# Kernel tuning notes

Hardware: AMD Instinct MI355X
Metric: run time of the kernel (lower is better)

Reference implementation:

```python
import jax, jax.numpy as jnp
import numpy as np

N_NODES = 100000
N_EDGES = 1600000
HIDDEN = 64
N_MID = 3  # num_layers=5 -> 1 first + 3 middle + 1 last


def setup_inputs() -> dict:
    key = jax.random.key(0)
    ks = jax.random.split(key, 12)
    x = jax.random.normal(ks[0], (N_NODES, 1), dtype=jnp.float32)
    edge_index = jax.random.randint(ks[1], (2, N_EDGES), 0, N_NODES, dtype=jnp.int32)
    edge_weight = jax.random.uniform(ks[2], (N_EDGES,), dtype=jnp.float32)
    s0 = 1.0  # fan_in=1
    sh = 1.0 / np.sqrt(HIDDEN)
    Wrel0 = jax.random.normal(ks[3], (HIDDEN, 1), dtype=jnp.float32) * s0
    brel0 = jax.random.normal(ks[4], (HIDDEN,), dtype=jnp.float32) * s0
    Wroot0 = jax.random.normal(ks[5], (HIDDEN, 1), dtype=jnp.float32) * s0
    Wrel_mid = jax.random.normal(ks[6], (N_MID, HIDDEN, HIDDEN), dtype=jnp.float32) * sh
    brel_mid = jax.random.normal(ks[7], (N_MID, HIDDEN), dtype=jnp.float32) * sh
    Wroot_mid = jax.random.normal(ks[8], (N_MID, HIDDEN, HIDDEN), dtype=jnp.float32) * sh
    WrelL = jax.random.normal(ks[9], (1, HIDDEN), dtype=jnp.float32) * sh
    brelL = jax.random.normal(ks[10], (1,), dtype=jnp.float32) * sh
    WrootL = jax.random.normal(ks[11], (1, HIDDEN), dtype=jnp.float32) * sh
    return {"x": x, "edge_index": edge_index, "edge_weight": edge_weight,
            "Wrel0": Wrel0, "brel0": brel0, "Wroot0": Wroot0,
            "Wrel_mid": Wrel_mid, "brel_mid": brel_mid, "Wroot_mid": Wroot_mid,
            "WrelL": WrelL, "brelL": brelL, "WrootL": WrootL}


def reference(x, edge_index, edge_weight, Wrel0, brel0, Wroot0,
              Wrel_mid, brel_mid, Wroot_mid, WrelL, brelL, WrootL):
    src = edge_index[0]
    dst = edge_index[1]
    n = x.shape[0]

    def conv(h, Wrel, brel, Wroot):
        # PyG GraphConv(aggr='add'): lin_rel(sum_j w_ij * h_j) + lin_root(h_i)
        msg = h[src] * edge_weight[:, None]          # [E, C]
        agg = jax.ops.segment_sum(msg, dst, num_segments=n)  # [N, C]
        return agg @ Wrel.T + brel + h @ Wroot.T

    # dropout omitted (deterministic reference); relu after all but last layer
    h = jax.nn.relu(conv(x, Wrel0, brel0, Wroot0))
    for i in range(Wrel_mid.shape[0]):
        h = jax.nn.relu(conv(h, Wrel_mid[i], brel_mid[i], Wroot_mid[i]))
    return conv(h, WrelL, brelL, WrootL)  # [N, 1]
```

## Files before the change

### kernel.cpp

```cpp
#include <hip/hip_runtime.h>
#include <stdint.h>


#define NN 100000
#define NE 1600000
#define HID 64
#define NBKT 391
#define CAP 8192
#define PMAX (NBKT * CAP)
#define TILE 4096
#define EPT 16
#define NTILE ((NE + TILE - 1) / TILE)

typedef __attribute__((ext_vector_type(8))) short bf16x8;
typedef __attribute__((ext_vector_type(4))) float f32x4;
typedef __attribute__((ext_vector_type(2))) unsigned int u32x2;
typedef __attribute__((ext_vector_type(4))) unsigned int u32x4;

__device__ __forceinline__ uint32_t rne_bf16(float v) {
    uint32_t u = __float_as_uint(v);
    return (u + 0x7fffu + ((u >> 16) & 1u)) >> 16;
}


__global__ __launch_bounds__(256) void k_bpart(const int* __restrict__ src,
                                               const int* __restrict__ dst,
                                               const float* __restrict__ w,
                                               int* __restrict__ bcur,
                                               int2* __restrict__ bpairs) {
    __shared__ int  hcnt[NBKT];
    __shared__ int  hoff[NBKT];
    __shared__ int  hadj[NBKT];
    __shared__ int  sc0[512];
    __shared__ int  sc1[512];
    __shared__ int2 sT[TILE];
    __shared__ int  sAdj[TILE];
    int tile0 = blockIdx.x * TILE;
    int t = threadIdx.x;
    for (int i = t; i < NBKT; i += 256) hcnt[i] = 0;
    __syncthreads();

    int   pk[EPT];
    int   bk[EPT];
    float wv[EPT];
    #pragma unroll
    for (int k = 0; k < EPT; k++) {
        int e = tile0 + t + k * 256;
        if (e < NE) {
            int d = dst[e];
            int b = d >> 8;
            pk[k] = (src[e] << 8) | (d & 255);
            wv[k] = w[e];
            bk[k] = b;
            atomicAdd(&hcnt[b], 1);
        } else {
            bk[k] = -1;
        }
    }
    __syncthreads();

    sc0[t]       = (t < NBKT) ? hcnt[t] : 0;
    sc0[t + 256] = (t + 256 < NBKT) ? hcnt[t + 256] : 0;
    __syncthreads();
    int* cur = sc0;
    int* oth = sc1;
    for (int off = 1; off < 512; off <<= 1) {
        int v0 = cur[t]       + ((t       >= off) ? cur[t - off]       : 0);
        int v1 = cur[t + 256] + ((t + 256 >= off) ? cur[t + 256 - off] : 0);
        oth[t] = v0;
        oth[t + 256] = v1;
        __syncthreads();
        int* tmp = cur; cur = oth; oth = tmp;
    }
    for (int i = t; i < NBKT; i += 256) {
        int c = hcnt[i];
        int excl = cur[i] - c;
        hoff[i] = excl;
        int gbase = c ? atomicAdd(&bcur[i], c) : 0;
        hadj[i] = gbase - excl;
        hcnt[i] = 0;
    }
    __syncthreads();

    #pragma unroll
    for (int k = 0; k < EPT; k++) {
        if (bk[k] >= 0) {
            int b = bk[k];
            int pos = hoff[b] + atomicAdd(&hcnt[b], 1);
            sT[pos] = make_int2(pk[k], __float_as_int(wv[k]));
            sAdj[pos] = hadj[b];
        }
    }
    __syncthreads();

    int n = NE - tile0; if (n > TILE) n = TILE;
    for (int j = t; j < n; j += 256)
        bpairs[sAdj[j] + j] = sT[j];
}

__global__ __launch_bounds__(256) void k_bcsr(const int* __restrict__ bcur,
                                              const int2* __restrict__ bpairs,
                                              int* __restrict__ offs,
                                              int* __restrict__ ends,
                                              uint32_t* __restrict__ pairs) {
    __shared__ int2 sE[CAP];
    __shared__ int cnt[256];
    __shared__ int scn[256];
    __shared__ int cur[256];
    int k = blockIdx.x, t = threadIdx.x;
    int base = k * CAP;
    int scnt = bcur[k] - base;
    cnt[t] = 0;
    __syncthreads();
    for (int j = t; j < scnt; j += 256) {
        int2 q = bpairs[base + j];
        sE[j] = q;
        atomicAdd(&cnt[q.x & 255], 1);
    }
    __syncthreads();
    int v = cnt[t], acc = v;
    scn[t] = v;
    __syncthreads();
    for (int off = 1; off < 256; off <<= 1) {
        int u = (t >= off) ? scn[t - off] : 0;
        __syncthreads();
        acc += u;
        scn[t] = acc;
        __syncthreads();
    }
    int excl = acc - v;
    cur[t] = excl;
    int d = (k << 8) + t;
    if (d < NN) {
        offs[d] = base + excl;
        ends[d] = base + excl + v;
    }
    __syncthreads();
    for (int j = t; j < scnt; j += 256) {
        int2 q = sE[j];
        int pos = base + atomicAdd(&cur[q.x & 255], 1);
        uint32_t wb = rne_bf16(__int_as_float(q.y)) & 0x7fffu;
        pairs[pos] = (wb << 17) | (uint32_t)(q.x >> 8);
    }
}


__global__ __launch_bounds__(256) void k_wsplit(const float* __restrict__ Wrel_mid,
                                                const float* __restrict__ Wroot_mid,
                                                uint16_t* __restrict__ WgH,
                                                uint16_t* __restrict__ WgL,
                                                uint16_t* __restrict__ WrH,
                                                uint16_t* __restrict__ WrL,
                                                int* __restrict__ bcur) {
    int i = blockIdx.x * blockDim.x + threadIdx.x;
    if (i < NBKT) bcur[i] = i * CAP;
    if (i >= 3 * 4096) return;
    float a = Wrel_mid[i];
    uint32_t ah = rne_bf16(a);
    float al = a - __uint_as_float(ah << 16);
    WgH[i] = (uint16_t)ah;
    WgL[i] = (uint16_t)rne_bf16(al);
    float b = Wroot_mid[i];
    uint32_t bh = rne_bf16(b);
    float bl = b - __uint_as_float(bh << 16);
    WrH[i] = (uint16_t)bh;
    WrL[i] = (uint16_t)rne_bf16(bl);
}


__global__ __launch_bounds__(256) void k_l0pre(
        const int* __restrict__ offs, const int* __restrict__ ends,
        const uint32_t* __restrict__ pairs, const float* __restrict__ x,
        const float* __restrict__ Wrel0, const float* __restrict__ brel0,
        const float* __restrict__ Wroot0,
        uint16_t* __restrict__ Hout) {
    int c = threadIdx.x & 63;
    int w = threadIdx.x >> 6;
    int blk16 = blockIdx.x * 16;
    float agg[4];
    #pragma unroll
    for (int t = 0; t < 4; t++) {
        int node = blk16 + w * 4 + t;
        int b = offs[node], e = ends[node];
        float pp = 0.f;
        for (int j = b + c; j < e; j += 64) {
            uint32_t r = pairs[j];
            pp += __uint_as_float((r >> 17) << 16) * x[r & 0x1ffffu];
        }
        for (int o = 32; o > 0; o >>= 1) pp += __shfl_down(pp, o, 64);
        agg[t] = __shfl(pp, 0, 64);
    }
    float wr = Wrel0[c], br = brel0[c], wo = Wroot0[c];
    uint32_t* Hd = (uint32_t*)Hout;
    #pragma unroll
    for (int t = 0; t < 4; t++) {
        int node = blk16 + w * 4 + t;
        float v = agg[t] * wr + br + x[node] * wo;
        v = v > 0.f ? v : 0.f;
        uint32_t hb = rne_bf16(v);
        uint32_t pn = (uint32_t)__shfl_xor((int)hb, 1, 64);
        if (!(c & 1)) Hd[node * 32 + (c >> 1)] = hb | (pn << 16);
    }
}

#define TRRA(dst, off) \
    asm volatile("ds_read_b64_tr_b16 %0, %1 offset:" #off \
                 : "=v"(dst) : "v"(trbA))
#define TRRB(dst, off) \
    asm volatile("ds_read_b64_tr_b16 %0, %1 offset:" #off \
                 : "=v"(dst) : "v"(trbB))

template <bool LAST>
__global__ __launch_bounds__(64, 5) void k_aggfused(
        const int* __restrict__ offs, const int* __restrict__ ends,
        const uint32_t* __restrict__ pairs,
        const uint16_t* __restrict__ Hb,
        const uint16_t* __restrict__ WgH, const uint16_t* __restrict__ WgL,
        const uint16_t* __restrict__ WrH, const uint16_t* __restrict__ WrL,
        const float* __restrict__ brel,
        uint16_t* __restrict__ Hout,
        const float* __restrict__ WrelL, const float* __restrict__ WrootL,
        float* __restrict__ sarr, float* __restrict__ rarr) {
    __shared__ __align__(128) char smem[8192];
    int c = threadIdx.x;
    int n0 = blockIdx.x * 16;

    int myNode = n0 + (c & 15);
    int blo = offs[myNode];
    int bhi = ends[myNode];
    uint32_t wid = (uint32_t)(bhi - blo);
    int start  = __builtin_amdgcn_readlane(blo, 0);
    int finish = __builtin_amdgcn_readlane(bhi, 15);

    int kq = (c >> 4) * 8;
    int eprm  = ((c >> 5) << 2) | ((c >> 1) & 3);
    int lbyte = ((c >> 3) & 3) * 32 + (c & 1) * 16;
    char* stg = smem;
    uint32_t stgOff = (uint32_t)(uintptr_t)
        (__attribute__((address_space(3))) char*)stg;
    uint32_t trbA = stgOff + ((uint32_t)(c >> 4) << 10)
                          + ((uint32_t)(c & 15) << 3);
    uint32_t trbB = trbA + 4096;

    f32x4 acc16[4];
    #pragma unroll
    for (int nb = 0; nb < 4; nb++) acc16[nb] = f32x4{0.f, 0.f, 0.f, 0.f};

    const char* gbase = (const char*)Hb;
    int j0 = start + c; if (j0 > PMAX - 1) j0 = PMAX - 1;
    uint32_t praw = pairs[j0];
    uint32_t p = (start + c < finish) ? praw : 0;

    for (int cb = start; cb < finish; cb += 64) {
        int jn = cb + 64 + c; if (jn > PMAX - 1) jn = PMAX - 1;
        uint32_t pr2 = pairs[jn];
        #pragma unroll
        for (int i = 0; i < 4; i++) {
            uint32_t r = (uint32_t)__builtin_amdgcn_ds_bpermute(
                (eprm + i * 8) * 4, (int)p);
            uint32_t voff = ((r & 0x1ffffu) << 7) + (uint32_t)lbyte;
            __builtin_amdgcn_global_load_lds(
                (const __attribute__((address_space(1))) void*)(gbase + voff),
                (__attribute__((address_space(3))) void*)(stg + i * 1024),
                16, 0, 0);
        }
        #pragma unroll
        for (int i = 0; i < 4; i++) {
            uint32_t r = (uint32_t)__builtin_amdgcn_ds_bpermute(
                (32 + eprm + i * 8) * 4, (int)p);
            uint32_t voff = ((r & 0x1ffffu) << 7) + (uint32_t)lbyte;
            __builtin_amdgcn_global_load_lds(
                (const __attribute__((address_space(1))) void*)(gbase + voff),
                (__attribute__((address_space(3))) void*)(stg + 4096 + i * 1024),
                16, 0, 0);
        }
        uint32_t mA[8], mB[8];
        int dbA = cb + kq - blo;
        int dbB = cb + 32 + kq - blo;
        #pragma unroll
        for (int q = 0; q < 8; q++) {
            uint32_t rq = (uint32_t)__builtin_amdgcn_ds_bpermute(
                (kq + q) * 4, (int)p);
            mA[q] = ((uint32_t)(dbA + q) < wid) ? (rq >> 17) : 0u;
        }
        #pragma unroll
        for (int q = 0; q < 8; q++) {
            uint32_t rq = (uint32_t)__builtin_amdgcn_ds_bpermute(
                (32 + kq + q) * 4, (int)p);
            mB[q] = ((uint32_t)(dbB + q) < wid) ? (rq >> 17) : 0u;
        }
        u32x4 aav = { mA[0] | (mA[1] << 16), mA[2] | (mA[3] << 16),
                      mA[4] | (mA[5] << 16), mA[6] | (mA[7] << 16) };
        u32x4 abv = { mB[0] | (mB[1] << 16), mB[2] | (mB[3] << 16),
                      mB[4] | (mB[5] << 16), mB[6] | (mB[7] << 16) };
        bf16x8 afA = __builtin_bit_cast(bf16x8, aav);
        bf16x8 afB = __builtin_bit_cast(bf16x8, abv);
        asm volatile("s_waitcnt vmcnt(4)" ::: "memory");
        {
            u32x2 tb0, tb1, tb2, tb3, tb4, tb5, tb6, tb7;
            TRRA(tb0, 0);   TRRA(tb1, 512);
            TRRA(tb2, 128); TRRA(tb3, 640);
            TRRA(tb4, 256); TRRA(tb5, 768);
            TRRA(tb6, 384); TRRA(tb7, 896);
            asm volatile("s_waitcnt lgkmcnt(0)" ::: "memory");
            __builtin_amdgcn_sched_barrier(0);
            u32x4 bb0 = { tb0.x, tb0.y, tb1.x, tb1.y };
            acc16[0] = __builtin_amdgcn_mfma_f32_16x16x32_bf16(
                afA, __builtin_bit_cast(bf16x8, bb0), acc16[0], 0, 0, 0);
            u32x4 bb1 = { tb2.x, tb2.y, tb3.x, tb3.y };
            acc16[1] = __builtin_amdgcn_mfma_f32_16x16x32_bf16(
                afA, __builtin_bit_cast(bf16x8, bb1), acc16[1], 0, 0, 0);
            u32x4 bb2 = { tb4.x, tb4.y, tb5.x, tb5.y };
            acc16[2] = __builtin_amdgcn_mfma_f32_16x16x32_bf16(
                afA, __builtin_bit_cast(bf16x8, bb2), acc16[2], 0, 0, 0);
            u32x4 bb3 = { tb6.x, tb6.y, tb7.x, tb7.y };
            acc16[3] = __builtin_amdgcn_mfma_f32_16x16x32_bf16(
                afA, __builtin_bit_cast(bf16x8, bb3), acc16[3], 0, 0, 0);
        }
        asm volatile("s_waitcnt vmcnt(0)" ::: "memory");
        {
            u32x2 tb0, tb1, tb2, tb3, tb4, tb5, tb6, tb7;
            TRRB(tb0, 0);   TRRB(tb1, 512);
            TRRB(tb2, 128); TRRB(tb3, 640);
            TRRB(tb4, 256); TRRB(tb5, 768);
            TRRB(tb6, 384); TRRB(tb7, 896);
            asm volatile("s_waitcnt lgkmcnt(0)" ::: "memory");
            __builtin_amdgcn_sched_barrier(0);
            u32x4 bb0 = { tb0.x, tb0.y, tb1.x, tb1.y };
            acc16[0] = __builtin_amdgcn_mfma_f32_16x16x32_bf16(
                afB, __builtin_bit_cast(bf16x8, bb0), acc16[0], 0, 0, 0);
            u32x4 bb1 = { tb2.x, tb2.y, tb3.x, tb3.y };
            acc16[1] = __builtin_amdgcn_mfma_f32_16x16x32_bf16(
                afB, __builtin_bit_cast(bf16x8, bb1), acc16[1], 0, 0, 0);
            u32x4 bb2 = { tb4.x, tb4.y, tb5.x, tb5.y };
            acc16[2] = __builtin_amdgcn_mfma_f32_16x16x32_bf16(
                afB, __builtin_bit_cast(bf16x8, bb2), acc16[2], 0, 0, 0);
            u32x4 bb3 = { tb6.x, tb6.y, tb7.x, tb7.y };
            acc16[3] = __builtin_amdgcn_mfma_f32_16x16x32_bf16(
                afB, __builtin_bit_cast(bf16x8, bb3), acc16[3], 0, 0, 0);
        }
        p = (cb + 64 + c < finish) ? pr2 : 0;
    }
    asm volatile("s_waitcnt vmcnt(0)" ::: "memory");

    int row = c & 15;
    int quad = c >> 4;
    int kb = quad * 8;
    bf16x8 hs0 = *(const bf16x8*)&Hb[(n0 + row) * 64 + kb];
    bf16x8 hs1 = *(const bf16x8*)&Hb[(n0 + row) * 64 + 32 + kb];
    uint32_t* sHw = (uint32_t*)smem;
    #pragma unroll
    for (int t = 0; t < 4; t++) {
        #pragma unroll
        for (int nb = 0; nb < 4; nb++) {
            uint32_t hb = rne_bf16(acc16[nb][t]);
            uint32_t pn2 = (uint32_t)__shfl_xor((int)hb, 1, 64);
            if (!(c & 1))
                sHw[(quad * 4 + t) * 36 + nb * 8 + (row >> 1)]
                    = hb | (pn2 << 16);
        }
    }
    asm volatile("s_waitcnt lgkmcnt(0)" ::: "memory");
    __builtin_amdgcn_sched_barrier(0);
    bf16x8 ah0 = *(const bf16x8*)&sHw[row * 36 + quad * 4];
    bf16x8 ah1 = *(const bf16x8*)&sHw[row * 36 + 16 + quad * 4];

    if (!LAST) {
        uint16_t* sO = (uint16_t*)(smem + 2304);
        #pragma unroll
        for (int ob = 0; ob < 4; ob++) {
            int oc = ob * 16 + row;
            float bias = brel[oc];
            f32x4 acc = {bias, bias, bias, bias};
            bf16x8 gh0 = *(const bf16x8*)&WgH[oc * 64 + kb];
            bf16x8 gh1 = *(const bf16x8*)&WgH[oc * 64 + 32 + kb];
            bf16x8 gl0 = *(const bf16x8*)&WgL[oc * 64 + kb];
            bf16x8 gl1 = *(const bf16x8*)&WgL[oc * 64 + 32 + kb];
            acc = __builtin_amdgcn_mfma_f32_16x16x32_bf16(ah0, gh0, acc, 0, 0, 0);
            acc = __builtin_amdgcn_mfma_f32_16x16x32_bf16(ah1, gh1, acc, 0, 0, 0);
            acc = __builtin_amdgcn_mfma_f32_16x16x32_bf16(ah0, gl0, acc, 0, 0, 0);
            acc = __builtin_amdgcn_mfma_f32_16x16x32_bf16(ah1, gl1, acc, 0, 0, 0);
            bf16x8 rh0 = *(const bf16x8*)&WrH[oc * 64 + kb];
            bf16x8 rh1 = *(const bf16x8*)&WrH[oc * 64 + 32 + kb];
            bf16x8 rl0 = *(const bf16x8*)&WrL[oc * 64 + kb];
            bf16x8 rl1 = *(const bf16x8*)&WrL[oc * 64 + 32 + kb];
            acc = __builtin_amdgcn_mfma_f32_16x16x32_bf16(hs0, rh0, acc, 0, 0, 0);
            acc = __builtin_amdgcn_mfma_f32_16x16x32_bf16(hs1, rh1, acc, 0, 0, 0);
            acc = __builtin_amdgcn_mfma_f32_16x16x32_bf16(hs0, rl0, acc, 0, 0, 0);
            acc = __builtin_amdgcn_mfma_f32_16x16x32_bf16(hs1, rl1, acc, 0, 0, 0);
            #pragma unroll
            for (int r = 0; r < 4; r++) {
                float v = acc[r] > 0.f ? acc[r] : 0.f;
                sO[(quad * 4 + r) * 68 + oc] = (uint16_t)rne_bf16(v);
            }
        }
        asm volatile("s_waitcnt lgkmcnt(0)" ::: "memory");
        __builtin_amdgcn_sched_barrier(0);
        const uint32_t* sOd = (const uint32_t*)sO;
        uint32_t* Hd = (uint32_t*)Hout;
        #pragma unroll
        for (int it = 0; it < 8; it++) {
            int idx = it * 64 + c;
            int nd = idx >> 5, col = idx & 31;
            Hd[(n0 + nd) * 32 + col] = sOd[nd * 34 + col];
        }
    } else {
        float pa[4] = {0.f, 0.f, 0.f, 0.f};
        float pr[4] = {0.f, 0.f, 0.f, 0.f};
        #pragma unroll
        for (int ob = 0; ob < 4; ob++) {
            int oc = ob * 16 + row;
            float bias = brel[oc];
            f32x4 acc = {bias, bias, bias, bias};
            bf16x8 gh0 = *(const bf16x8*)&WgH[oc * 64 + kb];
            bf16x8 gh1 = *(const bf16x8*)&WgH[oc * 64 + 32 + kb];
            bf16x8 gl0 = *(const bf16x8*)&WgL[oc * 64 + kb];
            bf16x8 gl1 = *(const bf16x8*)&WgL[oc * 64 + 32 + kb];
            acc = __builtin_amdgcn_mfma_f32_16x16x32_bf16(ah0, gh0, acc, 0, 0, 0);
            acc = __builtin_amdgcn_mfma_f32_16x16x32_bf16(ah1, gh1, acc, 0, 0, 0);
            acc = __builtin_amdgcn_mfma_f32_16x16x32_bf16(ah0, gl0, acc, 0, 0, 0);
            acc = __builtin_amdgcn_mfma_f32_16x16x32_bf16(ah1, gl1, acc, 0, 0, 0);
            bf16x8 rh0 = *(const bf16x8*)&WrH[oc * 64 + kb];
            bf16x8 rh1 = *(const bf16x8*)&WrH[oc * 64 + 32 + kb];
            bf16x8 rl0 = *(const bf16x8*)&WrL[oc * 64 + kb];
            bf16x8 rl1 = *(const bf16x8*)&WrL[oc * 64 + 32 + kb];
            acc = __builtin_amdgcn_mfma_f32_16x16x32_bf16(hs0, rh0, acc, 0, 0, 0);
            acc = __builtin_amdgcn_mfma_f32_16x16x32_bf16(hs1, rh1, acc, 0, 0, 0);
            acc = __builtin_amdgcn_mfma_f32_16x16x32_bf16(hs0, rl0, acc, 0, 0, 0);
            acc = __builtin_amdgcn_mfma_f32_16x16x32_bf16(hs1, rl1, acc, 0, 0, 0);
            float wlc = WrelL[oc], woc = WrootL[oc];
            #pragma unroll
            for (int r = 0; r < 4; r++) {
                float v = acc[r] > 0.f ? acc[r] : 0.f;
                pa[r] += v * wlc;
                pr[r] += v * woc;
            }
        }
        #pragma unroll
        for (int r = 0; r < 4; r++) {
            #pragma unroll
            for (int o = 8; o > 0; o >>= 1) {
                pa[r] += __shfl_down(pa[r], o, 16);
                pr[r] += __shfl_down(pr[r], o, 16);
            }
            if (row == 0) {
                int node = n0 + quad * 4 + r;
                sarr[node] = pa[r];
                rarr[node] = pr[r];
            }
        }
    }
}

__global__ __launch_bounds__(256) void k_last(
        const int* __restrict__ offs, const int* __restrict__ ends,
        const uint32_t* __restrict__ pairs,
        const float* __restrict__ sarr, const float* __restrict__ rarr,
        const float* __restrict__ brelL, float* __restrict__ out) {
    int c = threadIdx.x & 63;
    int w = threadIdx.x >> 6;
    int blk16 = blockIdx.x * 16;
    float b0 = brelL[0];
    #pragma unroll
    for (int t = 0; t < 4; t++) {
        int node = blk16 + w * 4 + t;
        int b = offs[node], e = ends[node];
        float pp = 0.f;
        for (int j = b + c; j < e; j += 64) {
            uint32_t r = pairs[j];
            pp += __uint_as_float((r >> 17) << 16) * sarr[r & 0x1ffffu];
        }
        #pragma unroll
        for (int o = 32; o > 0; o >>= 1) pp += __shfl_down(pp, o, 64);
        if (c == 0) out[node] = pp + rarr[node] + b0;
    }
}

extern "C" void kernel_launch(void* const* d_in, const int* in_sizes, int n_in,
                              void* d_out, int out_size, void* d_ws, size_t ws_size,
                              hipStream_t stream) {
    const float* x        = (const float*)d_in[0];
    const int*   ei       = (const int*)d_in[1];
    const float* ew       = (const float*)d_in[2];
    const float* Wrel0    = (const float*)d_in[3];
    const float* brel0    = (const float*)d_in[4];
    const float* Wroot0   = (const float*)d_in[5];
    const float* Wrel_mid = (const float*)d_in[6];
    const float* brel_mid = (const float*)d_in[7];
    const float* Wroot_mid= (const float*)d_in[8];
    const float* WrelL    = (const float*)d_in[9];
    const float* brelL    = (const float*)d_in[10];
    const float* WrootL   = (const float*)d_in[11];
    float* out = (float*)d_out;

    const int* src  = ei;
    const int* dstp = ei + NE;

    char* w = (char*)d_ws;
    size_t o = 0;
    auto alloc = [&](size_t b) -> void* {
        void* r = (void*)(w + o);
        o += (b + 255) & ~(size_t)255;
        return r;
    };
    int*      offs  = (int*)alloc((size_t)NN * 4);
    int*      ends  = (int*)alloc((size_t)NN * 4);
    int*      bcur  = (int*)alloc((size_t)NBKT * 4);
    uint16_t* WgH   = (uint16_t*)alloc((size_t)3 * 4096 * 2);
    uint16_t* WgL   = (uint16_t*)alloc((size_t)3 * 4096 * 2);
    uint16_t* WrH   = (uint16_t*)alloc((size_t)3 * 4096 * 2);
    uint16_t* WrL   = (uint16_t*)alloc((size_t)3 * 4096 * 2);
    float*    sarr  = (float*)alloc((size_t)NN * 4);
    float*    rarr  = (float*)alloc((size_t)NN * 4);
    uint32_t* pairs = (uint32_t*)alloc((size_t)NBKT * CAP * 4);
    uint16_t* HbA   = (uint16_t*)alloc((size_t)NN * HID * 2);
    uint16_t* HbB   = (uint16_t*)alloc((size_t)NN * HID * 2);
    uint16_t* spare = (uint16_t*)alloc((size_t)NN * HID * 2);
    (void)spare;
    int2*  bpairs = (int2*)HbB;

    k_wsplit<<<(3 * 4096 + 255) / 256, 256, 0, stream>>>(
        Wrel_mid, Wroot_mid, WgH, WgL, WrH, WrL, bcur);

    k_bpart<<<NTILE, 256, 0, stream>>>(src, dstp, ew, bcur, bpairs);
    k_bcsr<<<NBKT, 256, 0, stream>>>(bcur, bpairs, offs, ends, pairs);

    k_l0pre<<<NN / 16, 256, 0, stream>>>(
        offs, ends, pairs, x, Wrel0, brel0, Wroot0, HbA);

    int nagg = NN / 16;
    k_aggfused<false><<<nagg, 64, 0, stream>>>(
        offs, ends, pairs, HbA,
        WgH, WgL, WrH, WrL, brel_mid,
        HbB, WrelL, WrootL, sarr, rarr);
    k_aggfused<false><<<nagg, 64, 0, stream>>>(
        offs, ends, pairs, HbB,
        WgH + 4096, WgL + 4096, WrH + 4096, WrL + 4096, brel_mid + HID,
        HbA, WrelL, WrootL, sarr, rarr);
    k_aggfused<true><<<nagg, 64, 0, stream>>>(
        offs, ends, pairs, HbA,
        WgH + 2 * 4096, WgL + 2 * 4096, WrH + 2 * 4096, WrL + 2 * 4096,
        brel_mid + 2 * HID,
        HbB, WrelL, WrootL, sarr, rarr);

    k_last<<<NN / 16, 256, 0, stream>>>(offs, ends, pairs, sarr, rarr, brelL, out);
}
```

Measured before the change: 288.5 us.

## Recompute layer-0 features on the fly inside first middle-layer aggregation

Layer 0 no longer writes a 64-wide bf16 hidden tensor. The pre-pass stores only the scalar aggregate and the input per node (8 bytes). A new first middle-layer kernel gathers those two scalars per edge and rebuilds the layer-0 ReLU features in registers before feeding the MFMA aggregation. This trades the 128-byte-per-edge gather and the 12.8MB write and read of layer-0 hidden states for extra ALU work and cross-lane permutes per edge.

```diff
diff --git a/kernel.cpp b/kernel.cpp
--- a/kernel.cpp
+++ b/kernel.cpp
@@ -171,13 +171,10 @@
 __global__ __launch_bounds__(256) void k_l0pre(
         const int* __restrict__ offs, const int* __restrict__ ends,
         const uint32_t* __restrict__ pairs, const float* __restrict__ x,
-        const float* __restrict__ Wrel0, const float* __restrict__ brel0,
-        const float* __restrict__ Wroot0,
-        uint16_t* __restrict__ Hout) {
+        float2* __restrict__ AX) {
     int c = threadIdx.x & 63;
     int w = threadIdx.x >> 6;
     int blk16 = blockIdx.x * 16;
-    float agg[4];
     #pragma unroll
     for (int t = 0; t < 4; t++) {
         int node = blk16 + w * 4 + t;
@@ -188,18 +185,7 @@
             pp += __uint_as_float((r >> 17) << 16) * x[r & 0x1ffffu];
         }
         for (int o = 32; o > 0; o >>= 1) pp += __shfl_down(pp, o, 64);
-        agg[t] = __shfl(pp, 0, 64);
-    }
-    float wr = Wrel0[c], br = brel0[c], wo = Wroot0[c];
-    uint32_t* Hd = (uint32_t*)Hout;
-    #pragma unroll
-    for (int t = 0; t < 4; t++) {
-        int node = blk16 + w * 4 + t;
-        float v = agg[t] * wr + br + x[node] * wo;
-        v = v > 0.f ? v : 0.f;
-        uint32_t hb = rne_bf16(v);
-        uint32_t pn = (uint32_t)__shfl_xor((int)hb, 1, 64);
-        if (!(c & 1)) Hd[node * 32 + (c >> 1)] = hb | (pn << 16);
+        if (c == 0) AX[node] = make_float2(pp, x[node]);
     }
 }
 
@@ -209,6 +195,179 @@
 #define TRRB(dst, off) \
     asm volatile("ds_read_b64_tr_b16 %0, %1 offset:" #off \
                  : "=v"(dst) : "v"(trbB))
+
+__global__ __launch_bounds__(64, 4) void k_agg1(
+        const int* __restrict__ offs, const int* __restrict__ ends,
+        const uint32_t* __restrict__ pairs,
+        const float2* __restrict__ AX,
+        const float* __restrict__ Wrel0, const float* __restrict__ brel0,
+        const float* __restrict__ Wroot0,
+        const uint16_t* __restrict__ WgH, const uint16_t* __restrict__ WgL,
+        const uint16_t* __restrict__ WrH, const uint16_t* __restrict__ WrL,
+        const float* __restrict__ brel,
+        uint16_t* __restrict__ Hout) {
+    __shared__ __align__(128) char smem[4608];
+    int c = threadIdx.x;
+    int n0 = blockIdx.x * 16;
+    int row = c & 15;
+    int quad = c >> 4;
+    int kq = quad * 8;
+
+    int myNode = n0 + row;
+    int blo = offs[myNode];
+    int bhi = ends[myNode];
+    uint32_t wid = (uint32_t)(bhi - blo);
+    int start  = __builtin_amdgcn_readlane(blo, 0);
+    int finish = __builtin_amdgcn_readlane(bhi, 15);
+
+    float wrc[4], brc[4], woc[4];
+    #pragma unroll
+    for (int nb = 0; nb < 4; nb++) {
+        int col = nb * 16 + row;
+        wrc[nb] = Wrel0[col]; brc[nb] = brel0[col]; woc[nb] = Wroot0[col];
+    }
+
+    f32x4 acc16[4];
+    #pragma unroll
+    for (int nb = 0; nb < 4; nb++) acc16[nb] = f32x4{0.f, 0.f, 0.f, 0.f};
+
+    int j0 = start + c; if (j0 > PMAX - 1) j0 = PMAX - 1;
+    uint32_t praw = pairs[j0];
+    uint32_t p = (start + c < finish) ? praw : 0;
+
+    for (int cb = start; cb < finish; cb += 64) {
+        int jn = cb + 64 + c; if (jn > PMAX - 1) jn = PMAX - 1;
+        uint32_t pr2 = pairs[jn];
+        float2 ax = AX[p & 0x1ffffu];
+        uint32_t mA[8], mB[8];
+        int dbA = cb + kq - blo;
+        int dbB = cb + 32 + kq - blo;
+        #pragma unroll
+        for (int q = 0; q < 8; q++) {
+            uint32_t rq = (uint32_t)__builtin_amdgcn_ds_bpermute(
+                (kq + q) * 4, (int)p);
+            mA[q] = ((uint32_t)(dbA + q) < wid) ? (rq >> 17) : 0u;
+        }
+        #pragma unroll
+        for (int q = 0; q < 8; q++) {
+            uint32_t rq = (uint32_t)__builtin_amdgcn_ds_bpermute(
+                (32 + kq + q) * 4, (int)p);
+            mB[q] = ((uint32_t)(dbB + q) < wid) ? (rq >> 17) : 0u;
+        }
+        u32x4 aav = { mA[0] | (mA[1] << 16), mA[2] | (mA[3] << 16),
+                      mA[4] | (mA[5] << 16), mA[6] | (mA[7] << 16) };
+        u32x4 abv = { mB[0] | (mB[1] << 16), mB[2] | (mB[3] << 16),
+                      mB[4] | (mB[5] << 16), mB[6] | (mB[7] << 16) };
+        bf16x8 afA = __builtin_bit_cast(bf16x8, aav);
+        bf16x8 afB = __builtin_bit_cast(bf16x8, abv);
+        asm volatile("s_waitcnt vmcnt(0)" ::: "memory");
+        int areg = __float_as_int(ax.x);
+        int xreg = __float_as_int(ax.y);
+        #pragma unroll
+        for (int s = 0; s < 2; s++) {
+            float av[8], xv[8];
+            #pragma unroll
+            for (int q = 0; q < 8; q++) {
+                int idx = (s * 32 + kq + q) * 4;
+                av[q] = __int_as_float(__builtin_amdgcn_ds_bpermute(idx, areg));
+                xv[q] = __int_as_float(__builtin_amdgcn_ds_bpermute(idx, xreg));
+            }
+            bf16x8 af = s ? afB : afA;
+            #pragma unroll
+            for (int nb = 0; nb < 4; nb++) {
+                uint32_t hh[8];
+                #pragma unroll
+                for (int q = 0; q < 8; q++) {
+                    float h = av[q] * wrc[nb] + brc[nb] + xv[q] * woc[nb];
+                    h = h > 0.f ? h : 0.f;
+                    hh[q] = rne_bf16(h);
+                }
+                u32x4 bb = { hh[0] | (hh[1] << 16), hh[2] | (hh[3] << 16),
+                             hh[4] | (hh[5] << 16), hh[6] | (hh[7] << 16) };
+                acc16[nb] = __builtin_amdgcn_mfma_f32_16x16x32_bf16(
+                    af, __builtin_bit_cast(bf16x8, bb), acc16[nb], 0, 0, 0);
+            }
+        }
+        p = (cb + 64 + c < finish) ? pr2 : 0;
+    }
+
+    float2 axs = AX[n0 + row];
+    uint32_t e0[8], e1[8];
+    #pragma unroll
+    for (int q = 0; q < 8; q++) {
+        int k0 = kq + q;
+        float h = axs.x * Wrel0[k0] + brel0[k0] + axs.y * Wroot0[k0];
+        h = h > 0.f ? h : 0.f;
+        e0[q] = rne_bf16(h);
+        int k1 = 32 + kq + q;
+        float h2 = axs.x * Wrel0[k1] + brel0[k1] + axs.y * Wroot0[k1];
+        h2 = h2 > 0.f ? h2 : 0.f;
+        e1[q] = rne_bf16(h2);
+    }
+    u32x4 hv0 = { e0[0] | (e0[1] << 16), e0[2] | (e0[3] << 16),
+                  e0[4] | (e0[5] << 16), e0[6] | (e0[7] << 16) };
+    u32x4 hv1 = { e1[0] | (e1[1] << 16), e1[2] | (e1[3] << 16),
+                  e1[4] | (e1[5] << 16), e1[6] | (e1[7] << 16) };
+    bf16x8 hs0 = __builtin_bit_cast(bf16x8, hv0);
+    bf16x8 hs1 = __builtin_bit_cast(bf16x8, hv1);
+
+    uint32_t* sHw = (uint32_t*)smem;
+    #pragma unroll
+    for (int t = 0; t < 4; t++) {
+        #pragma unroll
+        for (int nb = 0; nb < 4; nb++) {
+            uint32_t hb = rne_bf16(acc16[nb][t]);
+            uint32_t pn2 = (uint32_t)__shfl_xor((int)hb, 1, 64);
+            if (!(c & 1))
+                sHw[(quad * 4 + t) * 36 + nb * 8 + (row >> 1)]
+                    = hb | (pn2 << 16);
+        }
+    }
+    asm volatile("s_waitcnt lgkmcnt(0)" ::: "memory");
+    __builtin_amdgcn_sched_barrier(0);
+    int kb = quad * 8;
+    bf16x8 ah0 = *(const bf16x8*)&sHw[row * 36 + quad * 4];
+    bf16x8 ah1 = *(const bf16x8*)&sHw[row * 36 + 16 + quad * 4];
+
+    uint16_t* sO = (uint16_t*)(smem + 2304);
+    #pragma unroll
+    for (int ob = 0; ob < 4; ob++) {
+        int oc = ob * 16 + row;
+        float bias = brel[oc];
+        f32x4 acc = {bias, bias, bias, bias};
+        bf16x8 gh0 = *(const bf16x8*)&WgH[oc * 64 + kb];
+        bf16x8 gh1 = *(const bf16x8*)&WgH[oc * 64 + 32 + kb];
+        bf16x8 gl0 = *(const bf16x8*)&WgL[oc * 64 + kb];
+        bf16x8 gl1 = *(const bf16x8*)&WgL[oc * 64 + 32 + kb];
+        acc = __builtin_amdgcn_mfma_f32_16x16x32_bf16(ah0, gh0, acc, 0, 0, 0);
+        acc = __builtin_amdgcn_mfma_f32_16x16x32_bf16(ah1, gh1, acc, 0, 0, 0);
+        acc = __builtin_amdgcn_mfma_f32_16x16x32_bf16(ah0, gl0, acc, 0, 0, 0);
+        acc = __builtin_amdgcn_mfma_f32_16x16x32_bf16(ah1, gl1, acc, 0, 0, 0);
+        bf16x8 rh0 = *(const bf16x8*)&WrH[oc * 64 + kb];
+        bf16x8 rh1 = *(const bf16x8*)&WrH[oc * 64 + 32 + kb];
+        bf16x8 rl0 = *(const bf16x8*)&WrL[oc * 64 + kb];
+        bf16x8 rl1 = *(const bf16x8*)&WrL[oc * 64 + 32 + kb];
+        acc = __builtin_amdgcn_mfma_f32_16x16x32_bf16(hs0, rh0, acc, 0, 0, 0);
+        acc = __builtin_amdgcn_mfma_f32_16x16x32_bf16(hs1, rh1, acc, 0, 0, 0);
+        acc = __builtin_amdgcn_mfma_f32_16x16x32_bf16(hs0, rl0, acc, 0, 0, 0);
+        acc = __builtin_amdgcn_mfma_f32_16x16x32_bf16(hs1, rl1, acc, 0, 0, 0);
+        #pragma unroll
+        for (int r = 0; r < 4; r++) {
+            float v = acc[r] > 0.f ? acc[r] : 0.f;
+            sO[(quad * 4 + r) * 68 + oc] = (uint16_t)rne_bf16(v);
+        }
+    }
+    asm volatile("s_waitcnt lgkmcnt(0)" ::: "memory");
+    __builtin_amdgcn_sched_barrier(0);
+    const uint32_t* sOd = (const uint32_t*)sO;
+    uint32_t* Hd = (uint32_t*)Hout;
+    #pragma unroll
+    for (int it = 0; it < 8; it++) {
+        int idx = it * 64 + c;
+        int nd = idx >> 5, col = idx & 31;
+        Hd[(n0 + nd) * 32 + col] = sOd[nd * 34 + col];
+    }
+}
 
 template <bool LAST>
 __global__ __launch_bounds__(64, 5) void k_aggfused(
@@ -512,6 +671,7 @@
     uint16_t* WrL   = (uint16_t*)alloc((size_t)3 * 4096 * 2);
     float*    sarr  = (float*)alloc((size_t)NN * 4);
     float*    rarr  = (float*)alloc((size_t)NN * 4);
+    float2*   AX    = (float2*)alloc((size_t)NN * 8);
     uint32_t* pairs = (uint32_t*)alloc((size_t)NBKT * CAP * 4);
     uint16_t* HbA   = (uint16_t*)alloc((size_t)NN * HID * 2);
     uint16_t* HbB   = (uint16_t*)alloc((size_t)NN * HID * 2);
@@ -525,14 +685,12 @@
     k_bpart<<<NTILE, 256, 0, stream>>>(src, dstp, ew, bcur, bpairs);
     k_bcsr<<<NBKT, 256, 0, stream>>>(bcur, bpairs, offs, ends, pairs);
 
-    k_l0pre<<<NN / 16, 256, 0, stream>>>(
-        offs, ends, pairs, x, Wrel0, brel0, Wroot0, HbA);
+    k_l0pre<<<NN / 16, 256, 0, stream>>>(offs, ends, pairs, x, AX);
 
     int nagg = NN / 16;
-    k_aggfused<false><<<nagg, 64, 0, stream>>>(
-        offs, ends, pairs, HbA,
-        WgH, WgL, WrH, WrL, brel_mid,
-        HbB, WrelL, WrootL, sarr, rarr);
+    k_agg1<<<nagg, 64, 0, stream>>>(
+        offs, ends, pairs, AX, Wrel0, brel0, Wroot0,
+        WgH, WgL, WrH, WrL, brel_mid, HbB);
     k_aggfused<false><<<nagg, 64, 0, stream>>>(
         offs, ends, pairs, HbB,
         WgH + 4096, WgL + 4096, WrH + 4096, WrL + 4096, brel_mid + HID,
```

Measured after the change: 287.5 us. No clear change (-0.3%).
